# Optimization experiments

Hardware: AMD Instinct MI355X
Metric: run time of the kernel (lower is better)

The kernel has to match this reference:

```python
import jax, jax.numpy as jnp
import numpy as np

NUM_FIELDS = 40
# upper-triangular (i<j) field pair indices, computed once at trace time
_I_IDX, _J_IDX = np.triu_indices(NUM_FIELDS, k=1)  # each length 780


def setup_inputs() -> dict:
    key = jax.random.key(0)
    k1, k2 = jax.random.split(key)
    batch, num_fields, embed_dim = 8192, NUM_FIELDS, 32
    num_interactions = num_fields * (num_fields - 1) // 2  # 780
    embeddings = jax.random.normal(k1, (batch, num_fields, embed_dim), dtype=jnp.float32)
    W = jax.random.normal(k2, (num_interactions, embed_dim, embed_dim), dtype=jnp.float32)
    return {"embeddings": embeddings, "W": W}


def reference(embeddings, W):
    # embeddings: (b, f, e); W: (k, e, e) with k = f*(f-1)/2
    vi = embeddings[:, _I_IDX, :]  # (b, k, e)
    vj = embeddings[:, _J_IDX, :]  # (b, k, e)
    # per-pair bilinear form, reduced over embed dims -> (b, k)
    return jnp.einsum('bke,kef,bkf->bk', vi, W, vj)
```

## Files before the change

### kernel.cpp

```cpp
#include <hip/hip_runtime.h>
#include <cstdint>
#include <cstddef>

typedef __attribute__((ext_vector_type(8))) short short8;
typedef __attribute__((ext_vector_type(4))) unsigned short ushort4_t;
typedef __attribute__((ext_vector_type(16))) float f32x16;

#define NF 40
#define NK 780
#define BT 32
#define THREADS 1024

__device__ __forceinline__ unsigned short f2bf(float f) {
    unsigned int u = __float_as_uint(f);
    u = (u + 0x7fffu + ((u >> 16) & 1u)) >> 16;
    return (unsigned short)u;
}
__device__ __forceinline__ float bf2f(unsigned short x) {
    return __uint_as_float(((unsigned int)x) << 16);
}

__global__ __launch_bounds__(128) void wprep_kernel(const float* __restrict__ W,
                                                    unsigned short* __restrict__ wfrag) {
    const int k = blockIdx.x, t = threadIdx.x;
    const int half = t >> 6, l = t & 63;
    const int e = l & 31;
    const int f0 = 16 * half + 8 * (l >> 5);
    const float* src = W + (size_t)k * 1024 + e * 32 + f0;
    const float4 x0 = *(const float4*)src;
    const float4 x1 = *(const float4*)(src + 4);
    short8 v;
    v[0] = (short)f2bf(x0.x); v[1] = (short)f2bf(x0.y);
    v[2] = (short)f2bf(x0.z); v[3] = (short)f2bf(x0.w);
    v[4] = (short)f2bf(x1.x); v[5] = (short)f2bf(x1.y);
    v[6] = (short)f2bf(x1.z); v[7] = (short)f2bf(x1.w);
    *(short8*)(wfrag + (size_t)k * 1024 + half * 512 + l * 8) = v;
}

__device__ __forceinline__ void ld_w4(short8& r0, short8& r1, short8& r2, short8& r3,
                                      const char* addr) {
    asm volatile("global_load_dwordx4 %0, %4, off\n\t"
                 "global_load_dwordx4 %1, %4, off offset:1024\n\t"
                 "global_load_dwordx4 %2, %4, off offset:2048\n\t"
                 "global_load_dwordx4 %3, %4, off offset:3072"
                 : "=&v"(r0), "=&v"(r1), "=&v"(r2), "=&v"(r3)
                 : "v"(addr));
}
#define WAITP() do { asm volatile("s_waitcnt vmcnt(4)" ::: "memory"); \
                     __builtin_amdgcn_sched_barrier(0); } while (0)
#define WAIT0() do { asm volatile("s_waitcnt vmcnt(0)" ::: "memory"); \
                     __builtin_amdgcn_sched_barrier(0); } while (0)

#define LOADW2(R0, R1, R2, R3, KB)                                                      \
    {                                                                                   \
        const int kbc = (KB) > 778 ? 778 : (KB);                                        \
        ld_w4(R0, R1, R2, R3, wbase + ((size_t)kbc << 11));                             \
    }


#define RELOAD_VI()                                                                     \
    {                                                                                   \
        const int i7 = ii & 7;                                                          \
        const char* ibase = embT + (ii << 11) + eoff;                                   \
        const ushort4_t r0 = *(const ushort4_t*)(ibase + (((b32     ) ^ i7) << 4));     \
        const ushort4_t r1 = *(const ushort4_t*)(ibase + (((b32 + 32) ^ i7) << 4));     \
        const ushort4_t r2 = *(const ushort4_t*)(ibase + (((b32 + 64) ^ i7) << 4));     \
        const ushort4_t r3 = *(const ushort4_t*)(ibase + (((b32 + 96) ^ i7) << 4));     \
        vf0  = bf2f(r0[0]); vf1  = bf2f(r0[1]); vf2  = bf2f(r0[2]); vf3  = bf2f(r0[3]); \
        vf4  = bf2f(r1[0]); vf5  = bf2f(r1[1]); vf6  = bf2f(r1[2]); vf7  = bf2f(r1[3]); \
        vf8  = bf2f(r2[0]); vf9  = bf2f(r2[1]); vf10 = bf2f(r2[2]); vf11 = bf2f(r2[3]); \
        vf12 = bf2f(r3[0]); vf13 = bf2f(r3[1]); vf14 = bf2f(r3[2]); vf15 = bf2f(r3[3]); \
    }

#define KSTEP(A0, A1, OREG)                                                             \
    {                                                                                   \
        const int j7 = jj & 7;                                                          \
        const char* jbase = embT + (jj << 11);                                          \
        const short8 vj0 = *(const short8*)(jbase + (((b32 + fq0) ^ j7) << 4));         \
        const short8 vj1 = *(const short8*)(jbase + (((b32 + fq1) ^ j7) << 4));         \
        f32x16 t = __builtin_amdgcn_mfma_f32_32x32x16_bf16(A0, vj0, zacc, 0, 0, 0);     \
        t = __builtin_amdgcn_mfma_f32_32x32x16_bf16(A1, vj1, t, 0, 0, 0);               \
        float c0 = t[0] * vf0;                                                          \
        c0 = __builtin_fmaf(t[1], vf1, c0);                                             \
        c0 = __builtin_fmaf(t[2], vf2, c0);                                             \
        c0 = __builtin_fmaf(t[3], vf3, c0);                                             \
        float c1 = t[4] * vf4;                                                          \
        c1 = __builtin_fmaf(t[5], vf5, c1);                                             \
        c1 = __builtin_fmaf(t[6], vf6, c1);                                             \
        c1 = __builtin_fmaf(t[7], vf7, c1);                                             \
        float c2 = t[8] * vf8;                                                          \
        c2 = __builtin_fmaf(t[9], vf9, c2);                                             \
        c2 = __builtin_fmaf(t[10], vf10, c2);                                           \
        c2 = __builtin_fmaf(t[11], vf11, c2);                                           \
        float c3 = t[12] * vf12;                                                        \
        c3 = __builtin_fmaf(t[13], vf13, c3);                                           \
        c3 = __builtin_fmaf(t[14], vf14, c3);                                           \
        c3 = __builtin_fmaf(t[15], vf15, c3);                                           \
        float p = (c0 + c1) + (c2 + c3);                                                \
        p += __shfl_xor(p, 32);                                                         \
        OREG = p;                                                                       \
        ++jj;                                                                           \
        if (jj == NF) { ++ii; jj = ii + 1; RELOAD_VI(); }                               \
    }

#define STEP2(KNEXT, C0, C1, C2, C3, N0, N1, N2, N3, OA, OB)                            \
    LOADW2(N0, N1, N2, N3, KNEXT);                                                      \
    WAITP();                                                                            \
    KSTEP(C0, C1, OA);                                                                  \
    KSTEP(C2, C3, OB);

__global__ __launch_bounds__(THREADS, 4) void bil_kernel(const float* __restrict__ emb,
                                                         const unsigned short* __restrict__ wfrag,
                                                         float* __restrict__ out) {
    __shared__ __align__(16) char embT[NF * 2048];

    const int tid = threadIdx.x;
    const int b0 = blockIdx.x * BT;

    for (int u = tid; u < BT * 160; u += THREADS) {
        const int bb = u / 160;
        const int t = u - 160 * bb;
        const int field = t >> 2;
        const int fq = t & 3;
        const float* src = emb + (size_t)(b0 + bb) * (NF * 32) + field * 32 + 8 * fq;
        const float4 x0 = *(const float4*)src;
        const float4 x1 = *(const float4*)(src + 4);
        short8 v;
        v[0] = (short)f2bf(x0.x); v[1] = (short)f2bf(x0.y);
        v[2] = (short)f2bf(x0.z); v[3] = (short)f2bf(x0.w);
        v[4] = (short)f2bf(x1.x); v[5] = (short)f2bf(x1.y);
        v[6] = (short)f2bf(x1.z); v[7] = (short)f2bf(x1.w);
        const int g = (bb + 32 * fq) ^ (field & 7);
        *(short8*)(embT + field * 2048 + g * 16) = v;
    }
    __syncthreads();

    const int ww = tid >> 6;
    const int l = tid & 63;
    const int b32 = l & 31;
    const int h32 = l >> 5;
    const int fq0 = 32 * h32;
    const int fq1 = 64 + 32 * h32;
    const int eoff = 8 * h32;

    const f32x16 zacc = {};

    const int ks = 4 * ((195 * ww) >> 4);
    const int ke = 4 * ((195 * (ww + 1)) >> 4);

    int ii = 0, jj;
    {
        int kk = ks, len = 39;
        while (kk >= len) { kk -= len; ++ii; --len; }
        jj = ii + 1 + kk;
    }

    float vf0, vf1, vf2, vf3, vf4, vf5, vf6, vf7;
    float vf8, vf9, vf10, vf11, vf12, vf13, vf14, vf15;
    RELOAD_VI();

    const char* wbase = (const char*)wfrag + l * 16;

    short8 a0, a1, a2, a3;
    short8 bb0, bb1, bb2, bb3;
    LOADW2(a0, a1, a2, a3, ks);

    int kcur = ks;
    while (kcur + 16 <= ke) {
        float o0, o1, o2, o3, o4, o5, o6, o7;
        float o8, o9, o10, o11, o12, o13, o14, o15;
        STEP2(kcur + 2,  a0, a1, a2, a3, bb0, bb1, bb2, bb3, o0,  o1)
        STEP2(kcur + 4,  bb0, bb1, bb2, bb3, a0, a1, a2, a3, o2,  o3)
        STEP2(kcur + 6,  a0, a1, a2, a3, bb0, bb1, bb2, bb3, o4,  o5)
        STEP2(kcur + 8,  bb0, bb1, bb2, bb3, a0, a1, a2, a3, o6,  o7)
        STEP2(kcur + 10, a0, a1, a2, a3, bb0, bb1, bb2, bb3, o8,  o9)
        STEP2(kcur + 12, bb0, bb1, bb2, bb3, a0, a1, a2, a3, o10, o11)
        STEP2(kcur + 14, a0, a1, a2, a3, bb0, bb1, bb2, bb3, o12, o13)
        STEP2(kcur + 16, bb0, bb1, bb2, bb3, a0, a1, a2, a3, o14, o15)
        if (l < 32) {
            float* orow = out + (size_t)(b0 + l) * NK + kcur;
            float4 s;
            s.x = o0;  s.y = o1;  s.z = o2;  s.w = o3;  *(float4*)(orow)      = s;
            s.x = o4;  s.y = o5;  s.z = o6;  s.w = o7;  *(float4*)(orow + 4)  = s;
            s.x = o8;  s.y = o9;  s.z = o10; s.w = o11; *(float4*)(orow + 8)  = s;
            s.x = o12; s.y = o13; s.z = o14; s.w = o15; *(float4*)(orow + 12) = s;
        }
        kcur += 16;
    }
    if (kcur < ke) {
        float o0, o1, o2, o3;
        LOADW2(bb0, bb1, bb2, bb3, kcur + 2);
        WAITP();
        KSTEP(a0, a1, o0);
        KSTEP(a2, a3, o1);
        WAIT0();
        KSTEP(bb0, bb1, o2);
        KSTEP(bb2, bb3, o3);
        if (l < 32) {
            float4 s; s.x = o0; s.y = o1; s.z = o2; s.w = o3;
            *(float4*)(out + (size_t)(b0 + l) * NK + kcur) = s;
        }
    }
}

extern "C" void kernel_launch(void* const* d_in, const int* in_sizes, int n_in,
                              void* d_out, int out_size, void* d_ws, size_t ws_size,
                              hipStream_t stream) {
    const float* emb = (const float*)d_in[0];
    const float* W   = (const float*)d_in[1];
    float* out = (float*)d_out;
    unsigned short* wfrag = (unsigned short*)d_ws;

    wprep_kernel<<<dim3(NK), dim3(128), 0, stream>>>(W, wfrag);
    bil_kernel<<<dim3(8192 / BT), dim3(THREADS), 0, stream>>>(emb, wfrag, out);
}
```

Before: 41.81 us.

## Interleave interaction chunks across waves with round-robin 8-pair assignment

Each wave previously handled one contiguous range of about 48 interaction indices. Now each wave takes 8-pair chunks in round-robin order (chunk c = ww + 16m), and a closed-form sqrt-based index recovery sets (i,j) at the start of each chunk. At any moment the 16 waves then read adjacent W fragment regions, which may improve L2/cache locality and balance the tail. The cost is a per-chunk index recomputation, a reload of the vi registers, and a smaller unroll with more frequent narrower output stores.

```diff
diff --git a/kernel.cpp b/kernel.cpp
--- a/kernel.cpp
+++ b/kernel.cpp
@@ -103,11 +103,36 @@
         if (jj == NF) { ++ii; jj = ii + 1; RELOAD_VI(); }                               \
     }
 
-#define STEP2(KNEXT, C0, C1, C2, C3, N0, N1, N2, N3, OA, OB)                            \
-    LOADW2(N0, N1, N2, N3, KNEXT);                                                      \
-    WAITP();                                                                            \
-    KSTEP(C0, C1, OA);                                                                  \
-    KSTEP(C2, C3, OB);
+#define SETIJ(K)                                                                        \
+    {                                                                                   \
+        const int k_ = (K);                                                             \
+        int i_ = (int)((79.0f - __builtin_sqrtf((float)(6241 - 8 * k_))) * 0.5f);       \
+        if (i_ < 0) i_ = 0;                                                             \
+        while ((i_ + 1) * (78 - i_) / 2 <= k_) ++i_;                                    \
+        while (i_ * (79 - i_) / 2 > k_) --i_;                                           \
+        ii = i_;                                                                        \
+        jj = i_ + 1 + (k_ - i_ * (79 - i_) / 2);                                        \
+        RELOAD_VI();                                                                    \
+    }
+
+#define CHUNK8(K0, KNEXT)                                                               \
+    {                                                                                   \
+        float o0, o1, o2, o3, o4, o5, o6, o7;                                           \
+        LOADW2(bw0, bw1, bw2, bw3, (K0) + 2); WAITP();                                  \
+        KSTEP(aw0, aw1, o0); KSTEP(aw2, aw3, o1);                                       \
+        LOADW2(aw0, aw1, aw2, aw3, (K0) + 4); WAITP();                                  \
+        KSTEP(bw0, bw1, o2); KSTEP(bw2, bw3, o3);                                       \
+        LOADW2(bw0, bw1, bw2, bw3, (K0) + 6); WAITP();                                  \
+        KSTEP(aw0, aw1, o4); KSTEP(aw2, aw3, o5);                                       \
+        LOADW2(aw0, aw1, aw2, aw3, (KNEXT)); WAITP();                                   \
+        KSTEP(bw0, bw1, o6); KSTEP(bw2, bw3, o7);                                       \
+        if (l < 32) {                                                                   \
+            float* orow = out + orowbase + (K0);                                        \
+            float4 s;                                                                   \
+            s.x = o0; s.y = o1; s.z = o2; s.w = o3; *(float4*)orow = s;                 \
+            s.x = o4; s.y = o5; s.z = o6; s.w = o7; *(float4*)(orow + 4) = s;           \
+        }                                                                               \
+    }
 
 __global__ __launch_bounds__(THREADS, 4) void bil_kernel(const float* __restrict__ emb,
                                                          const unsigned short* __restrict__ wfrag,
@@ -145,60 +170,38 @@
 
     const f32x16 zacc = {};
 
-    const int ks = 4 * ((195 * ww) >> 4);
-    const int ke = 4 * ((195 * (ww + 1)) >> 4);
-
-    int ii = 0, jj;
-    {
-        int kk = ks, len = 39;
-        while (kk >= len) { kk -= len; ++ii; --len; }
-        jj = ii + 1 + kk;
-    }
-
+    int ii, jj;
     float vf0, vf1, vf2, vf3, vf4, vf5, vf6, vf7;
     float vf8, vf9, vf10, vf11, vf12, vf13, vf14, vf15;
-    RELOAD_VI();
 
     const char* wbase = (const char*)wfrag + l * 16;
-
-    short8 a0, a1, a2, a3;
-    short8 bb0, bb1, bb2, bb3;
-    LOADW2(a0, a1, a2, a3, ks);
-
-    int kcur = ks;
-    while (kcur + 16 <= ke) {
-        float o0, o1, o2, o3, o4, o5, o6, o7;
-        float o8, o9, o10, o11, o12, o13, o14, o15;
-        STEP2(kcur + 2,  a0, a1, a2, a3, bb0, bb1, bb2, bb3, o0,  o1)
-        STEP2(kcur + 4,  bb0, bb1, bb2, bb3, a0, a1, a2, a3, o2,  o3)
-        STEP2(kcur + 6,  a0, a1, a2, a3, bb0, bb1, bb2, bb3, o4,  o5)
-        STEP2(kcur + 8,  bb0, bb1, bb2, bb3, a0, a1, a2, a3, o6,  o7)
-        STEP2(kcur + 10, a0, a1, a2, a3, bb0, bb1, bb2, bb3, o8,  o9)
-        STEP2(kcur + 12, bb0, bb1, bb2, bb3, a0, a1, a2, a3, o10, o11)
-        STEP2(kcur + 14, a0, a1, a2, a3, bb0, bb1, bb2, bb3, o12, o13)
-        STEP2(kcur + 16, bb0, bb1, bb2, bb3, a0, a1, a2, a3, o14, o15)
-        if (l < 32) {
-            float* orow = out + (size_t)(b0 + l) * NK + kcur;
-            float4 s;
-            s.x = o0;  s.y = o1;  s.z = o2;  s.w = o3;  *(float4*)(orow)      = s;
-            s.x = o4;  s.y = o5;  s.z = o6;  s.w = o7;  *(float4*)(orow + 4)  = s;
-            s.x = o8;  s.y = o9;  s.z = o10; s.w = o11; *(float4*)(orow + 8)  = s;
-            s.x = o12; s.y = o13; s.z = o14; s.w = o15; *(float4*)(orow + 12) = s;
-        }
-        kcur += 16;
-    }
-    if (kcur < ke) {
+    const size_t orowbase = (size_t)(b0 + b32) * NK;
+
+    short8 aw0, aw1, aw2, aw3;
+    short8 bw0, bw1, bw2, bw3;
+
+    LOADW2(aw0, aw1, aw2, aw3, 8 * ww);
+    int c = ww;
+#pragma unroll 1
+    for (int m = 0; m < 6; ++m) {
+        const int k0 = 8 * c;
+        SETIJ(k0);
+        const int knext = (m < 5) ? (k0 + 128) : ((ww < 3) ? (768 + 4 * ww) : 768);
+        CHUNK8(k0, knext);
+        c += 16;
+    }
+    if (ww < 3) {
+        const int k0r = 768 + 4 * ww;
+        SETIJ(k0r);
         float o0, o1, o2, o3;
-        LOADW2(bb0, bb1, bb2, bb3, kcur + 2);
+        LOADW2(bw0, bw1, bw2, bw3, k0r + 2);
         WAITP();
-        KSTEP(a0, a1, o0);
-        KSTEP(a2, a3, o1);
+        KSTEP(aw0, aw1, o0); KSTEP(aw2, aw3, o1);
         WAIT0();
-        KSTEP(bb0, bb1, o2);
-        KSTEP(bb2, bb3, o3);
+        KSTEP(bw0, bw1, o2); KSTEP(bw2, bw3, o3);
         if (l < 32) {
             float4 s; s.x = o0; s.y = o1; s.z = o2; s.w = o3;
-            *(float4*)(out + (size_t)(b0 + l) * NK + kcur) = s;
+            *(float4*)(out + orowbase + k0r) = s;
         }
     }
 }
```

Result: no change. 41.77 us (-0.1%).
